# Kernel tuning notes

Measured on AMD Instinct MI355X. Metric: run time of the kernel, lower is better.

Reference implementation:

```python
import jax, jax.numpy as jnp
import numpy as np

B, C, H, W, L = 2, 64, 48, 48, 48
GH, GW, GL = 24, 24, 24  # gating signal at half resolution


def setup_inputs() -> dict:
    key = jax.random.key(0)
    k = jax.random.split(key, 6)
    x = jax.random.normal(k[0], (B, C, H, W, L), dtype=jnp.float32)
    g = jax.random.normal(k[1], (B, C, GH, GW, GL), dtype=jnp.float32)
    s = 1.0 / np.sqrt(C)
    W1 = jax.random.normal(k[2], (C, C), dtype=jnp.float32) * s  # conv1 1x1x1 weight (out,in)
    b1 = jax.random.normal(k[3], (C,), dtype=jnp.float32) * 0.01
    W2 = jax.random.normal(k[4], (C, C), dtype=jnp.float32) * s  # conv2 1x1x1 weight
    b2 = jax.random.normal(k[5], (C,), dtype=jnp.float32) * 0.01
    return {"x": x, "g": g, "W1": W1, "b1": b1, "W2": W2, "b2": b2}


def _conv1x1(v, Wm, b):
    # 1x1x1 Conv3d == channel-mixing matmul
    return jnp.einsum('bchwl,oc->bohwl', v, Wm) + b[None, :, None, None, None]


def reference(x, g, W1, b1, W2, b2):
    theta_x = _conv1x1(x, W1, b1)                       # (B, C, H, W, L)
    theta_g = _conv1x1(g, W2, b2)                       # (B, C, GH, GW, GL)
    # F.upsample(mode='trilinear', align_corners=False) -> half-pixel trilinear resize
    theta_g = jax.image.resize(theta_g, (B, C, H, W, L), method='trilinear')

    # spatially-normalized elementwise gate
    theta_c = theta_x * theta_g
    theta_c = theta_c - jnp.min(theta_c)                # global min over whole tensor
    theta_c = theta_c / jnp.sum(theta_c, axis=(2, 3, 4), keepdims=True)
    p = theta_c * x

    # channel-channel attention per (b,h,w), contracting over L
    theta_c_d = jnp.einsum('bihwl,bjhwl->bhwij', theta_x, theta_g)  # (B,H,W,C,C)
    theta_c_d = theta_c_d - jnp.min(theta_c_d)
    theta_c_d = theta_c_d / jnp.sum(theta_c_d, axis=(1, 2, 3, 4), keepdims=True)
    d = jnp.einsum('bchwl,bhwcj->bjhwl', x, theta_c_d)  # (B, C, H, W, L)
    return (p, d)
```

## Files before the change

kernel.cpp:

```cpp
#include <hip/hip_runtime.h>

#define Bb 2
#define Cc 64
#define Hh 48
#define Ww 48
#define Ll 48
#define HWc (Hh*Ww)
#define HWL (HWc*Ll)
#define GHh 24
#define SG (GHh*GHh*GHh)
#define NBLK (Bb*HWc)
#define CNT1f 110592.0f
#define CNT2f 9437184.0f

__device__ __forceinline__ void interp1(int i, int& a, int& b, float& f){
  float src = i*0.5f - 0.25f;
  float fl = floorf(src);
  f = src - fl;
  int i0 = (int)fl;
  a = i0 < 0 ? 0 : i0;
  int i1 = i0 + 1;
  b = i1 > (GHh-1) ? (GHh-1) : i1;
}

__global__ __launch_bounds__(256) void conv_k(const float* __restrict__ in,
    const float* __restrict__ Wm, const float* __restrict__ bias,
    float* __restrict__ out, int S){
  __shared__ __align__(16) float Wl[64][68];
  __shared__ __align__(16) float xl[64][68];
  int t = threadIdx.x;
  int ntile = S >> 6;
  int b  = blockIdx.x / ntile;
  int s0 = (blockIdx.x % ntile) << 6;
  for (int q = t; q < 4096; q += 256){
    int o = q >> 6, c = q & 63;
    Wl[c][o] = Wm[q];
  }
  const float* inb = in + (size_t)b*Cc*S + s0;
  for (int q = t; q < 1024; q += 256){
    int c = q >> 4, v = (q & 15) << 2;
    float4 val = *(const float4*)(inb + (size_t)c*S + v);
    *(float4*)&xl[c][v] = val;
  }
  __syncthreads();
  int o0 = (t & 15) << 2, s1 = (t >> 4) << 2;
  float a00=0,a01=0,a02=0,a03=0,a10=0,a11=0,a12=0,a13=0;
  float a20=0,a21=0,a22=0,a23=0,a30=0,a31=0,a32=0,a33=0;
  #pragma unroll 8
  for (int c = 0; c < 64; ++c){
    float4 wv = *(const float4*)&Wl[c][o0];
    float4 xv = *(const float4*)&xl[c][s1];
    a00 += wv.x*xv.x; a01 += wv.x*xv.y; a02 += wv.x*xv.z; a03 += wv.x*xv.w;
    a10 += wv.y*xv.x; a11 += wv.y*xv.y; a12 += wv.y*xv.z; a13 += wv.y*xv.w;
    a20 += wv.z*xv.x; a21 += wv.z*xv.y; a22 += wv.z*xv.z; a23 += wv.z*xv.w;
    a30 += wv.w*xv.x; a31 += wv.w*xv.y; a32 += wv.w*xv.z; a33 += wv.w*xv.w;
  }
  float* ob = out + (size_t)b*Cc*S + s0 + s1;
  float b0 = bias[o0+0], b1v = bias[o0+1], b2v = bias[o0+2], b3 = bias[o0+3];
  { float4 r = make_float4(a00+b0,a01+b0,a02+b0,a03+b0); *(float4*)(ob + (size_t)(o0+0)*S) = r; }
  { float4 r = make_float4(a10+b1v,a11+b1v,a12+b1v,a13+b1v); *(float4*)(ob + (size_t)(o0+1)*S) = r; }
  { float4 r = make_float4(a20+b2v,a21+b2v,a22+b2v,a23+b2v); *(float4*)(ob + (size_t)(o0+2)*S) = r; }
  { float4 r = make_float4(a30+b3,a31+b3,a32+b3,a33+b3); *(float4*)(ob + (size_t)(o0+3)*S) = r; }
}

__device__ __forceinline__ void g_fold(const float* __restrict__ txt,
    float* __restrict__ G, int t){
  int c = t >> 2, kb = (t & 3)*6;
  const float* T = &txt[c*52];
  #pragma unroll
  for (int i = 0; i < 6; ++i){
    int k = kb + i;
    float v;
    if (k == 0)       v = T[0] + 0.75f*T[1] + 0.25f*T[2];
    else if (k == 23) v = 0.25f*T[45] + 0.75f*T[46] + T[47];
    else              v = 0.25f*T[2*k-1] + 0.75f*T[2*k]
                        + 0.75f*T[2*k+1] + 0.25f*T[2*k+2];
    G[k*68 + c] = v;
  }
}

__device__ __forceinline__ void gather_m(const float* __restrict__ gb,
    float* __restrict__ M, int t, int ha, int hb, int wa, int wb,
    float fh, float fw){
  float omh = 1.f - fh, omw = 1.f - fw;
  for (int u = t; u < 384; u += 256){
    int c = u / 6, s4 = (u % 6) << 2;
    const float* gc = gb + (size_t)c*SG;
    float4 vaa = *(const float4*)(gc + ha*576 + wa*24 + s4);
    float4 vba = *(const float4*)(gc + hb*576 + wa*24 + s4);
    float4 vab = *(const float4*)(gc + ha*576 + wb*24 + s4);
    float4 vbb = *(const float4*)(gc + hb*576 + wb*24 + s4);
    M[(s4+0)*68 + c] = omw*(omh*vaa.x + fh*vba.x) + fw*(omh*vab.x + fh*vbb.x);
    M[(s4+1)*68 + c] = omw*(omh*vaa.y + fh*vba.y) + fw*(omh*vab.y + fh*vbb.y);
    M[(s4+2)*68 + c] = omw*(omh*vaa.z + fh*vba.z) + fw*(omh*vab.z + fh*vbb.z);
    M[(s4+3)*68 + c] = omw*(omh*vaa.w + fh*vba.w) + fw*(omh*vab.w + fh*vbb.w);
  }
}

__global__ __launch_bounds__(256) void reduce_k(const float* __restrict__ tx,
    const float* __restrict__ tgh, float* __restrict__ part_row,
    float* __restrict__ pm1, float* __restrict__ pm2, float* __restrict__ ps2){
  __shared__ __align__(16) float sh[7224];
  float* txt = sh;
  float* M   = sh + 3328;
  float* G   = sh + 4960;
  float* red = sh + 6592;
  float* CM  = sh + 7104;
  float* SX  = sh + 7128;
  float* sxg = sh + 7176;
  int t = threadIdx.x;
  int bIdx = blockIdx.x;
  int b = bIdx / HWc, hw = bIdx % HWc;
  int h = hw / Ww, w = hw % Ww;
  int ha, hb; float fh; interp1(h, ha, hb, fh);
  int wa, wb; float fw; interp1(w, wa, wb, fw);
  const float* txb = tx + ((size_t)b*Cc*HWc + hw)*Ll;
  #pragma unroll
  for (int k = 0; k < 3; ++k){
    int q = t + (k << 8);
    int c = q / 12, v = (q % 12) << 2;
    *(float4*)&txt[c*52+v] = *(const float4*)(txb + (size_t)c*HWL + v);
  }
  gather_m(tgh + (size_t)b*Cc*SG, M, t, ha, hb, wa, wb, fh, fw);
  __syncthreads();
  g_fold(txt, G, t);
  if (t < 24){
    float s = 0.f;
    #pragma unroll 8
    for (int c = 0; c < 64; ++c) s += M[t*68 + c];
    CM[t] = s;
  }
  if (t >= 192 && t < 240){
    int l = t - 192;
    float s = 0.f;
    #pragma unroll 8
    for (int c = 0; c < 64; ++c) s += txt[c*52 + l];
    SX[l] = s;
  }
  __syncthreads();
  int c = t & 63, lg = t >> 6;
  float pmin = 3.4e38f;
  const float* Trow = &txt[c*52];
  #pragma unroll
  for (int li = 0; li < 12; ++li){
    int l = lg*12 + li;
    int la, lb; float fl; interp1(l, la, lb, fl);
    float tgv = (1.f-fl)*M[la*68 + c] + fl*M[lb*68 + c];
    pmin = fminf(pmin, Trow[l]*tgv);
  }
  if (t < 48){
    int la, lb; float fl; interp1(t, la, lb, fl);
    sxg[t] = SX[t] * ((1.f-fl)*CM[la] + fl*CM[lb]);
  }
  int i0 = (t & 15) << 2, j0 = (t >> 4) << 2;
  float a00=0,a01=0,a02=0,a03=0,a10=0,a11=0,a12=0,a13=0;
  float a20=0,a21=0,a22=0,a23=0,a30=0,a31=0,a32=0,a33=0;
  #pragma unroll 4
  for (int k = 0; k < 24; ++k){
    float4 gv = *(const float4*)&G[k*68 + i0];
    float4 mv = *(const float4*)&M[k*68 + j0];
    a00 += gv.x*mv.x; a01 += gv.x*mv.y; a02 += gv.x*mv.z; a03 += gv.x*mv.w;
    a10 += gv.y*mv.x; a11 += gv.y*mv.y; a12 += gv.y*mv.z; a13 += gv.y*mv.w;
    a20 += gv.z*mv.x; a21 += gv.z*mv.y; a22 += gv.z*mv.z; a23 += gv.z*mv.w;
    a30 += gv.w*mv.x; a31 += gv.w*mv.y; a32 += gv.w*mv.z; a33 += gv.w*mv.w;
  }
  float amin = fminf(fminf(fminf(a00,a01),fminf(a02,a03)),
               fminf(fminf(fminf(a10,a11),fminf(a12,a13)),
               fminf(fminf(fminf(a20,a21),fminf(a22,a23)),
                     fminf(fminf(a30,a31),fminf(a32,a33)))));
  if ((t & 15) == (t >> 4)){
    float* pr = part_row + (size_t)bIdx*64 + i0;
    pr[0] = a00; pr[1] = a11; pr[2] = a22; pr[3] = a33;
  }
  red[t] = pmin; red[256+t] = amin;
  __syncthreads();
  if (t < 128){
    red[t] = fminf(red[t], red[t+128]);
    red[256+t] = fminf(red[256+t], red[384+t]);
  }
  __syncthreads();
  if (t < 64){
    float v1 = fminf(red[t], red[t+64]);
    float v2 = fminf(red[256+t], red[320+t]);
    #pragma unroll
    for (int off = 32; off; off >>= 1){
      v1 = fminf(v1, __shfl_down(v1, off));
      v2 = fminf(v2, __shfl_down(v2, off));
    }
    if (t == 0){
      pm1[bIdx] = v1; pm2[bIdx] = v2;
      float tot = 0.f;
      #pragma unroll
      for (int l = 0; l < 48; ++l) tot += sxg[l];
      ps2[bIdx] = tot;
    }
  }
}

__global__ __launch_bounds__(256) void reduce2_k(const float* __restrict__ part_row,
    const float* __restrict__ pm1, const float* __restrict__ pm2,
    const float* __restrict__ ps2, float* __restrict__ rowsum,
    float* __restrict__ gmin, float* __restrict__ s2v){
  __shared__ float red[512];
  int t = threadIdx.x, blk = blockIdx.x;
  if (blk < 128){
    int b = blk >> 6, c = blk & 63;
    const float* src = part_row + (size_t)b*HWc*64 + c;
    float s = 0.f;
    #pragma unroll
    for (int k = 0; k < 9; ++k){
      int i = t + (k << 8);
      s += src[(size_t)i*64];
    }
    red[t] = s; __syncthreads();
    for (int sgap = 128; sgap >= 64; sgap >>= 1){
      if (t < sgap) red[t] += red[t+sgap];
      __syncthreads();
    }
    if (t < 64){
      float v = red[t];
      #pragma unroll
      for (int off = 32; off; off >>= 1) v += __shfl_down(v, off);
      if (t == 0) rowsum[blk] = v;
    }
  } else if (blk == 128){
    float m1 = 3.4e38f, m2 = 3.4e38f;
    for (int i = t; i < NBLK; i += 256){ m1 = fminf(m1, pm1[i]); m2 = fminf(m2, pm2[i]); }
    red[t] = m1; red[256+t] = m2; __syncthreads();
    for (int s = 128; s >= 1; s >>= 1){
      if (t < s){ red[t] = fminf(red[t], red[t+s]); red[256+t] = fminf(red[256+t], red[256+t+s]); }
      __syncthreads();
    }
    if (t == 0){ gmin[0] = red[0]; gmin[1] = red[256]; }
  } else {
    float sa = 0.f, sb = 0.f;
    for (int i = t; i < HWc; i += 256){ sa += ps2[i]; sb += ps2[HWc + i]; }
    red[t] = sa; red[256+t] = sb; __syncthreads();
    for (int s = 128; s >= 1; s >>= 1){
      if (t < s){ red[t] += red[t+s]; red[256+t] += red[256+t+s]; }
      __syncthreads();
    }
    if (t == 0){ s2v[0] = red[0]; s2v[1] = red[256]; }
  }
}

__global__ __launch_bounds__(256) void final_k(const float* __restrict__ x,
    const float* __restrict__ tx, const float* __restrict__ tgh,
    const float* __restrict__ gmin, const float* __restrict__ rowsum,
    const float* __restrict__ s2v, float* __restrict__ outp, float* __restrict__ outd){
  __shared__ __align__(16) float sh[10032];
  float* txt = sh;
  float* xs  = sh + 3328;
  float* M   = sh + 6656;
  float* G   = sh + 8288;
  float* iv1 = sh + 9920;
  float* Xs  = sh + 9984;
  int t = threadIdx.x;
  int bIdx = blockIdx.x;
  int b = bIdx / HWc, hw = bIdx % HWc;
  int h = hw / Ww, w = hw % Ww;
  int ha, hb; float fh; interp1(h, ha, hb, fh);
  int wa, wb; float fw; interp1(w, wa, wb, fw);
  size_t sbase = ((size_t)b*Cc*HWc + hw)*Ll;
  const float* txb = tx + sbase;
  const float* xb  = x  + sbase;
  float m1 = gmin[0], m2 = gmin[1];
  #pragma unroll
  for (int k = 0; k < 3; ++k){
    int q = t + (k << 8);
    int c = q / 12, v = (q % 12) << 2;
    *(float4*)&txt[c*52+v] = *(const float4*)(txb + (size_t)c*HWL + v);
    *(float4*)&xs [c*52+v] = *(const float4*)(xb  + (size_t)c*HWL + v);
  }
  gather_m(tgh + (size_t)b*Cc*SG, M, t, ha, hb, wa, wb, fh, fw);
  __syncthreads();
  g_fold(txt, G, t);
  if (t < 64) iv1[t] = 1.f/(rowsum[b*64 + t] - m1*CNT1f);
  if (t >= 192 && t < 240){
    int l = t - 192;
    float s = 0.f;
    #pragma unroll 8
    for (int c = 0; c < 64; ++c) s += xs[c*52 + l];
    Xs[l] = s;
  }
  float invd2 = 1.f/(s2v[b] - m2*CNT2f);
  __syncthreads();
  #pragma unroll
  for (int k = 0; k < 3; ++k){
    int q = t + (k << 8);
    int c = q / 12, l4 = (q % 12) << 2;
    float4 a  = *(const float4*)&txt[c*52+l4];
    float4 xv = *(const float4*)&xs [c*52+l4];
    float s = iv1[c];
    float4 r;
    {
      int la, lb; float fl; interp1(l4+0, la, lb, fl);
      float tgv = (1.f-fl)*M[la*68+c] + fl*M[lb*68+c];
      r.x = (a.x*tgv - m1)*s*xv.x;
    }
    {
      int la, lb; float fl; interp1(l4+1, la, lb, fl);
      float tgv = (1.f-fl)*M[la*68+c] + fl*M[lb*68+c];
      r.y = (a.y*tgv - m1)*s*xv.y;
    }
    {
      int la, lb; float fl; interp1(l4+2, la, lb, fl);
      float tgv = (1.f-fl)*M[la*68+c] + fl*M[lb*68+c];
      r.z = (a.z*tgv - m1)*s*xv.z;
    }
    {
      int la, lb; float fl; interp1(l4+3, la, lb, fl);
      float tgv = (1.f-fl)*M[la*68+c] + fl*M[lb*68+c];
      r.w = (a.w*tgv - m1)*s*xv.w;
    }
    *(float4*)(outp + sbase + (size_t)c*HWL + l4) = r;
  }
  __syncthreads();
  float* P = txt;
  if (t < 192){
    int k0 = t >> 3, l0 = (t & 7)*6;
    float c0=0,c1=0,c2=0,c3=0,c4=0,c5=0;
    const float* Gr = &G[k0*68];
    #pragma unroll 8
    for (int i = 0; i < 64; ++i){
      float gv = Gr[i];
      const float* xr = &xs[i*52 + l0];
      c0 += gv*xr[0]; c1 += gv*xr[1]; c2 += gv*xr[2];
      c3 += gv*xr[3]; c4 += gv*xr[4]; c5 += gv*xr[5];
    }
    float* pr = &P[k0*52 + l0];
    pr[0]=c0; pr[1]=c1; pr[2]=c2; pr[3]=c3; pr[4]=c4; pr[5]=c5;
  }
  __syncthreads();
  {
    int j0 = (t >> 4) << 2, l0 = (t & 15)*3;
    float d00=0,d01=0,d02=0,d10=0,d11=0,d12=0;
    float d20=0,d21=0,d22=0,d30=0,d31=0,d32=0;
    #pragma unroll 4
    for (int k = 0; k < 24; ++k){
      float4 mv = *(const float4*)&M[k*68 + j0];
      const float* pr = &P[k*52 + l0];
      float p0 = pr[0], p1 = pr[1], p2 = pr[2];
      d00 += mv.x*p0; d01 += mv.x*p1; d02 += mv.x*p2;
      d10 += mv.y*p0; d11 += mv.y*p1; d12 += mv.y*p2;
      d20 += mv.z*p0; d21 += mv.z*p1; d22 += mv.z*p2;
      d30 += mv.w*p0; d31 += mv.w*p1; d32 += mv.w*p2;
    }
    float x0 = m2*Xs[l0+0], x1 = m2*Xs[l0+1], x2 = m2*Xs[l0+2];
    float* o0 = outd + sbase + (size_t)(j0+0)*HWL + l0;
    float* o1 = outd + sbase + (size_t)(j0+1)*HWL + l0;
    float* o2 = outd + sbase + (size_t)(j0+2)*HWL + l0;
    float* o3 = outd + sbase + (size_t)(j0+3)*HWL + l0;
    o0[0]=(d00-x0)*invd2; o0[1]=(d01-x1)*invd2; o0[2]=(d02-x2)*invd2;
    o1[0]=(d10-x0)*invd2; o1[1]=(d11-x1)*invd2; o1[2]=(d12-x2)*invd2;
    o2[0]=(d20-x0)*invd2; o2[1]=(d21-x1)*invd2; o2[2]=(d22-x2)*invd2;
    o3[0]=(d30-x0)*invd2; o3[1]=(d31-x1)*invd2; o3[2]=(d32-x2)*invd2;
  }
}

extern "C" void kernel_launch(void* const* d_in, const int* in_sizes, int n_in,
                              void* d_out, int out_size, void* d_ws, size_t ws_size,
                              hipStream_t stream){
  (void)in_sizes; (void)n_in; (void)out_size; (void)ws_size;
  const float* x  = (const float*)d_in[0];
  const float* g  = (const float*)d_in[1];
  const float* W1 = (const float*)d_in[2];
  const float* b1 = (const float*)d_in[3];
  const float* W2 = (const float*)d_in[4];
  const float* b2 = (const float*)d_in[5];
  float* outp = (float*)d_out;
  float* outd = outp + (size_t)Bb*Cc*HWL;
  float* ws   = (float*)d_ws;
  float* txw    = ws;
  float* tghw   = txw + (size_t)Bb*Cc*HWL;
  float* part_row = tghw + (size_t)Bb*Cc*SG;
  float* pm1 = part_row + (size_t)NBLK*64;
  float* pm2 = pm1 + NBLK;
  float* ps2 = pm2 + NBLK;
  float* rowsum = ps2 + NBLK;
  float* gmin = rowsum + 128;
  float* s2v  = gmin + 2;

  hipLaunchKernelGGL(conv_k, dim3(Bb*(SG/64)), dim3(256), 0, stream, g, W2, b2, tghw, SG);
  hipLaunchKernelGGL(conv_k, dim3(Bb*(HWL/64)), dim3(256), 0, stream, x, W1, b1, txw, HWL);
  hipLaunchKernelGGL(reduce_k, dim3(NBLK), dim3(256), 0, stream, txw, tghw,
                     part_row, pm1, pm2, ps2);
  hipLaunchKernelGGL(reduce2_k, dim3(130), dim3(256), 0, stream, part_row, pm1, pm2, ps2,
                     rowsum, gmin, s2v);
  hipLaunchKernelGGL(final_k, dim3(NBLK), dim3(256), 0, stream, x, txw, tghw,
                     gmin, rowsum, s2v, outp, outd);
}
```

Baseline: 310.7 us.

## Fuse full-resolution conv1 into reduce and final kernels, recomputing theta_x per site

Drops the separate conv_k launch that wrote theta_x (about 28 MB) to the workspace. Both reduce_k and final_k now load x and a transposed copy of W1 into shared memory and recompute the 64x48 channel-mixing matmul for each (b,h,w) site. The global write and the two later reads of theta_x go away. In exchange each site does the conv twice, uses more shared memory per block (which may lower occupancy), and adds extra barriers.

```diff
diff --git a/kernel.cpp b/kernel.cpp
--- a/kernel.cpp
+++ b/kernel.cpp
@@ -61,22 +61,6 @@
   { float4 r = make_float4(a10+b1v,a11+b1v,a12+b1v,a13+b1v); *(float4*)(ob + (size_t)(o0+1)*S) = r; }
   { float4 r = make_float4(a20+b2v,a21+b2v,a22+b2v,a23+b2v); *(float4*)(ob + (size_t)(o0+2)*S) = r; }
   { float4 r = make_float4(a30+b3,a31+b3,a32+b3,a33+b3); *(float4*)(ob + (size_t)(o0+3)*S) = r; }
-}
-
-__device__ __forceinline__ void g_fold(const float* __restrict__ txt,
-    float* __restrict__ G, int t){
-  int c = t >> 2, kb = (t & 3)*6;
-  const float* T = &txt[c*52];
-  #pragma unroll
-  for (int i = 0; i < 6; ++i){
-    int k = kb + i;
-    float v;
-    if (k == 0)       v = T[0] + 0.75f*T[1] + 0.25f*T[2];
-    else if (k == 23) v = 0.25f*T[45] + 0.75f*T[46] + T[47];
-    else              v = 0.25f*T[2*k-1] + 0.75f*T[2*k]
-                        + 0.75f*T[2*k+1] + 0.25f*T[2*k+2];
-    G[k*68 + c] = v;
-  }
 }
 
 __device__ __forceinline__ void gather_m(const float* __restrict__ gb,
@@ -97,50 +81,107 @@
   }
 }
 
-__global__ __launch_bounds__(256) void reduce_k(const float* __restrict__ tx,
+__device__ __forceinline__ void g_fold(const float* __restrict__ txt,
+    float* __restrict__ G, int t){
+  int c = t >> 2, kb = (t & 3)*6;
+  const float* T = &txt[c*72];
+  #pragma unroll
+  for (int i = 0; i < 6; ++i){
+    int k = kb + i;
+    float v;
+    if (k == 0)       v = T[0] + 0.75f*T[1] + 0.25f*T[2];
+    else if (k == 23) v = 0.25f*T[45] + 0.75f*T[46] + T[47];
+    else              v = 0.25f*T[2*k-1] + 0.75f*T[2*k]
+                        + 0.75f*T[2*k+1] + 0.25f*T[2*k+2];
+    G[k*68 + c] = v;
+  }
+}
+
+__device__ __forceinline__ void site_conv(const float* __restrict__ xs,
+    const float* __restrict__ Wl, const float* __restrict__ b1,
+    int c0, int l0, float4 acc[4]){
+  acc[0] = make_float4(0.f,0.f,0.f,0.f);
+  acc[1] = make_float4(0.f,0.f,0.f,0.f);
+  acc[2] = make_float4(0.f,0.f,0.f,0.f);
+  acc[3] = make_float4(0.f,0.f,0.f,0.f);
+  #pragma unroll 8
+  for (int cc = 0; cc < 64; ++cc){
+    float4 wv = *(const float4*)&Wl[cc*72 + c0];
+    float4 xv = *(const float4*)&xs[cc*52 + l0];
+    acc[0].x += wv.x*xv.x; acc[0].y += wv.x*xv.y; acc[0].z += wv.x*xv.z; acc[0].w += wv.x*xv.w;
+    acc[1].x += wv.y*xv.x; acc[1].y += wv.y*xv.y; acc[1].z += wv.y*xv.z; acc[1].w += wv.y*xv.w;
+    acc[2].x += wv.z*xv.x; acc[2].y += wv.z*xv.y; acc[2].z += wv.z*xv.z; acc[2].w += wv.z*xv.w;
+    acc[3].x += wv.w*xv.x; acc[3].y += wv.w*xv.y; acc[3].z += wv.w*xv.z; acc[3].w += wv.w*xv.w;
+  }
+  float b0 = b1[c0+0], bb1 = b1[c0+1], b2 = b1[c0+2], b3 = b1[c0+3];
+  acc[0].x += b0;  acc[0].y += b0;  acc[0].z += b0;  acc[0].w += b0;
+  acc[1].x += bb1; acc[1].y += bb1; acc[1].z += bb1; acc[1].w += bb1;
+  acc[2].x += b2;  acc[2].y += b2;  acc[2].z += b2;  acc[2].w += b2;
+  acc[3].x += b3;  acc[3].y += b3;  acc[3].z += b3;  acc[3].w += b3;
+}
+
+__global__ __launch_bounds__(256) void reduce_k(const float* __restrict__ x,
+    const float* __restrict__ W1, const float* __restrict__ b1,
     const float* __restrict__ tgh, float* __restrict__ part_row,
     float* __restrict__ pm1, float* __restrict__ pm2, float* __restrict__ ps2){
-  __shared__ __align__(16) float sh[7224];
-  float* txt = sh;
-  float* M   = sh + 3328;
-  float* G   = sh + 4960;
-  float* red = sh + 6592;
-  float* CM  = sh + 7104;
-  float* SX  = sh + 7128;
-  float* sxg = sh + 7176;
+  __shared__ __align__(16) float sh[11832];
+  float* xs  = sh;
+  float* Wt  = sh + 3328;
+  float* M   = sh + 7936;
+  float* G   = sh + 9568;
+  float* red = sh + 11200;
+  float* CM  = sh + 11712;
+  float* SX  = sh + 11736;
+  float* sxg = sh + 11784;
   int t = threadIdx.x;
   int bIdx = blockIdx.x;
   int b = bIdx / HWc, hw = bIdx % HWc;
   int h = hw / Ww, w = hw % Ww;
   int ha, hb; float fh; interp1(h, ha, hb, fh);
   int wa, wb; float fw; interp1(w, wa, wb, fw);
-  const float* txb = tx + ((size_t)b*Cc*HWc + hw)*Ll;
+  const float* xb = x + ((size_t)b*Cc*HWc + hw)*Ll;
   #pragma unroll
   for (int k = 0; k < 3; ++k){
     int q = t + (k << 8);
     int c = q / 12, v = (q % 12) << 2;
-    *(float4*)&txt[c*52+v] = *(const float4*)(txb + (size_t)c*HWL + v);
+    *(float4*)&xs[c*52+v] = *(const float4*)(xb + (size_t)c*HWL + v);
+  }
+  for (int q = t; q < 4096; q += 256){
+    int o = q >> 6, c = q & 63;
+    Wt[c*72 + o] = W1[q];
   }
   gather_m(tgh + (size_t)b*Cc*SG, M, t, ha, hb, wa, wb, fh, fw);
   __syncthreads();
-  g_fold(txt, G, t);
-  if (t < 24){
+  int c0 = (t & 15) << 2, l0q = (t >> 4) << 2;
+  float4 acc[4];
+  if (t < 192) site_conv(xs, Wt, b1, c0, l0q, acc);
+  if (t >= 192 && t < 216){
+    int k = t - 192;
     float s = 0.f;
     #pragma unroll 8
-    for (int c = 0; c < 64; ++c) s += M[t*68 + c];
-    CM[t] = s;
-  }
+    for (int c = 0; c < 64; ++c) s += M[k*68 + c];
+    CM[k] = s;
+  }
+  __syncthreads();
+  if (t < 192){
+    *(float4*)&Wt[(c0+0)*72 + l0q] = acc[0];
+    *(float4*)&Wt[(c0+1)*72 + l0q] = acc[1];
+    *(float4*)&Wt[(c0+2)*72 + l0q] = acc[2];
+    *(float4*)&Wt[(c0+3)*72 + l0q] = acc[3];
+  }
+  __syncthreads();
+  g_fold(Wt, G, t);
   if (t >= 192 && t < 240){
     int l = t - 192;
     float s = 0.f;
     #pragma unroll 8
-    for (int c = 0; c < 64; ++c) s += txt[c*52 + l];
+    for (int c = 0; c < 64; ++c) s += Wt[c*72 + l];
     SX[l] = s;
   }
   __syncthreads();
   int c = t & 63, lg = t >> 6;
   float pmin = 3.4e38f;
-  const float* Trow = &txt[c*52];
+  const float* Trow = &Wt[c*72];
   #pragma unroll
   for (int li = 0; li < 12; ++li){
     int l = lg*12 + li;
@@ -245,16 +286,17 @@
 }
 
 __global__ __launch_bounds__(256) void final_k(const float* __restrict__ x,
-    const float* __restrict__ tx, const float* __restrict__ tgh,
-    const float* __restrict__ gmin, const float* __restrict__ rowsum,
-    const float* __restrict__ s2v, float* __restrict__ outp, float* __restrict__ outd){
-  __shared__ __align__(16) float sh[10032];
-  float* txt = sh;
-  float* xs  = sh + 3328;
-  float* M   = sh + 6656;
-  float* G   = sh + 8288;
-  float* iv1 = sh + 9920;
-  float* Xs  = sh + 9984;
+    const float* __restrict__ W1, const float* __restrict__ b1,
+    const float* __restrict__ tgh, const float* __restrict__ gmin,
+    const float* __restrict__ rowsum, const float* __restrict__ s2v,
+    float* __restrict__ outp, float* __restrict__ outd){
+  __shared__ __align__(16) float sh[11312];
+  float* xs  = sh;
+  float* Wt  = sh + 3328;
+  float* M   = sh + 7936;
+  float* G   = sh + 9568;
+  float* iv1 = sh + 11200;
+  float* Xs  = sh + 11264;
   int t = threadIdx.x;
   int bIdx = blockIdx.x;
   int b = bIdx / HWc, hw = bIdx % HWc;
@@ -262,20 +304,25 @@
   int ha, hb; float fh; interp1(h, ha, hb, fh);
   int wa, wb; float fw; interp1(w, wa, wb, fw);
   size_t sbase = ((size_t)b*Cc*HWc + hw)*Ll;
-  const float* txb = tx + sbase;
-  const float* xb  = x  + sbase;
+  const float* xb = x + sbase;
   float m1 = gmin[0], m2 = gmin[1];
   #pragma unroll
   for (int k = 0; k < 3; ++k){
     int q = t + (k << 8);
     int c = q / 12, v = (q % 12) << 2;
-    *(float4*)&txt[c*52+v] = *(const float4*)(txb + (size_t)c*HWL + v);
-    *(float4*)&xs [c*52+v] = *(const float4*)(xb  + (size_t)c*HWL + v);
+    *(float4*)&xs[c*52+v] = *(const float4*)(xb + (size_t)c*HWL + v);
+  }
+  for (int q = t; q < 4096; q += 256){
+    int o = q >> 6, c = q & 63;
+    Wt[c*72 + o] = W1[q];
   }
   gather_m(tgh + (size_t)b*Cc*SG, M, t, ha, hb, wa, wb, fh, fw);
-  __syncthreads();
-  g_fold(txt, G, t);
   if (t < 64) iv1[t] = 1.f/(rowsum[b*64 + t] - m1*CNT1f);
+  float invd2 = 1.f/(s2v[b] - m2*CNT2f);
+  __syncthreads();
+  int c0 = (t & 15) << 2, l0q = (t >> 4) << 2;
+  float4 acc[4];
+  if (t < 192) site_conv(xs, Wt, b1, c0, l0q, acc);
   if (t >= 192 && t < 240){
     int l = t - 192;
     float s = 0.f;
@@ -283,14 +330,22 @@
     for (int c = 0; c < 64; ++c) s += xs[c*52 + l];
     Xs[l] = s;
   }
-  float invd2 = 1.f/(s2v[b] - m2*CNT2f);
+  __syncthreads();
+  if (t < 192){
+    *(float4*)&Wt[(c0+0)*72 + l0q] = acc[0];
+    *(float4*)&Wt[(c0+1)*72 + l0q] = acc[1];
+    *(float4*)&Wt[(c0+2)*72 + l0q] = acc[2];
+    *(float4*)&Wt[(c0+3)*72 + l0q] = acc[3];
+  }
+  __syncthreads();
+  g_fold(Wt, G, t);
   __syncthreads();
   #pragma unroll
   for (int k = 0; k < 3; ++k){
     int q = t + (k << 8);
     int c = q / 12, l4 = (q % 12) << 2;
-    float4 a  = *(const float4*)&txt[c*52+l4];
-    float4 xv = *(const float4*)&xs [c*52+l4];
+    float4 a  = *(const float4*)&Wt[c*72+l4];
+    float4 xv = *(const float4*)&xs[c*52+l4];
     float s = iv1[c];
     float4 r;
     {
@@ -316,20 +371,20 @@
     *(float4*)(outp + sbase + (size_t)c*HWL + l4) = r;
   }
   __syncthreads();
-  float* P = txt;
+  float* P = Wt;
   if (t < 192){
     int k0 = t >> 3, l0 = (t & 7)*6;
-    float c0=0,c1=0,c2=0,c3=0,c4=0,c5=0;
+    float p0=0,p1=0,p2=0,p3=0,p4=0,p5=0;
     const float* Gr = &G[k0*68];
     #pragma unroll 8
     for (int i = 0; i < 64; ++i){
       float gv = Gr[i];
       const float* xr = &xs[i*52 + l0];
-      c0 += gv*xr[0]; c1 += gv*xr[1]; c2 += gv*xr[2];
-      c3 += gv*xr[3]; c4 += gv*xr[4]; c5 += gv*xr[5];
+      p0 += gv*xr[0]; p1 += gv*xr[1]; p2 += gv*xr[2];
+      p3 += gv*xr[3]; p4 += gv*xr[4]; p5 += gv*xr[5];
     }
     float* pr = &P[k0*52 + l0];
-    pr[0]=c0; pr[1]=c1; pr[2]=c2; pr[3]=c3; pr[4]=c4; pr[5]=c5;
+    pr[0]=p0; pr[1]=p1; pr[2]=p2; pr[3]=p3; pr[4]=p4; pr[5]=p5;
   }
   __syncthreads();
   {
@@ -371,8 +426,7 @@
   float* outp = (float*)d_out;
   float* outd = outp + (size_t)Bb*Cc*HWL;
   float* ws   = (float*)d_ws;
-  float* txw    = ws;
-  float* tghw   = txw + (size_t)Bb*Cc*HWL;
+  float* tghw   = ws;
   float* part_row = tghw + (size_t)Bb*Cc*SG;
   float* pm1 = part_row + (size_t)NBLK*64;
   float* pm2 = pm1 + NBLK;
@@ -382,11 +436,10 @@
   float* s2v  = gmin + 2;
 
   hipLaunchKernelGGL(conv_k, dim3(Bb*(SG/64)), dim3(256), 0, stream, g, W2, b2, tghw, SG);
-  hipLaunchKernelGGL(conv_k, dim3(Bb*(HWL/64)), dim3(256), 0, stream, x, W1, b1, txw, HWL);
-  hipLaunchKernelGGL(reduce_k, dim3(NBLK), dim3(256), 0, stream, txw, tghw,
+  hipLaunchKernelGGL(reduce_k, dim3(NBLK), dim3(256), 0, stream, x, W1, b1, tghw,
                      part_row, pm1, pm2, ps2);
   hipLaunchKernelGGL(reduce2_k, dim3(130), dim3(256), 0, stream, part_row, pm1, pm2, ps2,
                      rowsum, gmin, s2v);
-  hipLaunchKernelGGL(final_k, dim3(NBLK), dim3(256), 0, stream, x, txw, tghw,
+  hipLaunchKernelGGL(final_k, dim3(NBLK), dim3(256), 0, stream, x, W1, b1, tghw,
                      gmin, rowsum, s2v, outp, outd);
 }
```

Measured after the change: 317.4 us. 1.02x slower.

## Cache per-site interpolated gate and folded G from reduce kernel for final kernel

Applied to the files above, without the earlier changes.

The reduce kernel now writes its per-(b,h,w) interpolated gate matrix M and folded G matrix to workspace. The final kernel loads them instead of re-gathering the gating tensor and recomputing the fold. The final kernel also reads theta_x directly from global memory rather than staging it in shared memory, and uses closed-form L-axis interpolation weights (0.25/0.75). This cuts recomputation and shared memory use in the final kernel at the cost of about 2x1536 floats of extra global writes and reads per site. The reduce loop's L index is also rotated by channel, likely to spread shared-memory bank accesses.

```diff
diff --git a/kernel.cpp b/kernel.cpp
--- a/kernel.cpp
+++ b/kernel.cpp
@@ -21,6 +21,13 @@
   a = i0 < 0 ? 0 : i0;
   int i1 = i0 + 1;
   b = i1 > (GHh-1) ? (GHh-1) : i1;
+}
+
+__device__ __forceinline__ void ltaps(int l, int& a, int& b, float& f){
+  int i0 = (l - 1) >> 1;
+  a = i0 < 0 ? 0 : i0;
+  b = i0 + 1 > 23 ? 23 : i0 + 1;
+  f = (l & 1) ? 0.25f : 0.75f;
 }
 
 __global__ __launch_bounds__(256) void conv_k(const float* __restrict__ in,
@@ -98,7 +105,8 @@
 }
 
 __global__ __launch_bounds__(256) void reduce_k(const float* __restrict__ tx,
-    const float* __restrict__ tgh, float* __restrict__ part_row,
+    const float* __restrict__ tgh, float* __restrict__ msite,
+    float* __restrict__ gsite, float* __restrict__ part_row,
     float* __restrict__ pm1, float* __restrict__ pm2, float* __restrict__ ps2){
   __shared__ __align__(16) float sh[7224];
   float* txt = sh;
@@ -143,14 +151,28 @@
   const float* Trow = &txt[c*52];
   #pragma unroll
   for (int li = 0; li < 12; ++li){
-    int l = lg*12 + li;
-    int la, lb; float fl; interp1(l, la, lb, fl);
+    int l0r = lg*12 + li + c;
+    int l = l0r >= 96 ? l0r - 96 : (l0r >= 48 ? l0r - 48 : l0r);
+    int la, lb; float fl; ltaps(l, la, lb, fl);
     float tgv = (1.f-fl)*M[la*68 + c] + fl*M[lb*68 + c];
     pmin = fminf(pmin, Trow[l]*tgv);
   }
   if (t < 48){
-    int la, lb; float fl; interp1(t, la, lb, fl);
+    int la, lb; float fl; ltaps(t, la, lb, fl);
     sxg[t] = SX[t] * ((1.f-fl)*CM[la] + fl*CM[lb]);
+  }
+  float* msb = msite + (size_t)bIdx*1536;
+  float* gsb = gsite + (size_t)bIdx*1536;
+  for (int u = t; u < 384; u += 256){
+    int k = u >> 4, c4 = (u & 15) << 2;
+    float4 mv;
+    mv.x = M[k*68+c4+0]; mv.y = M[k*68+c4+1];
+    mv.z = M[k*68+c4+2]; mv.w = M[k*68+c4+3];
+    *(float4*)(msb + (u << 2)) = mv;
+    float4 gv;
+    gv.x = G[k*68+c4+0]; gv.y = G[k*68+c4+1];
+    gv.z = G[k*68+c4+2]; gv.w = G[k*68+c4+3];
+    *(float4*)(gsb + (u << 2)) = gv;
   }
   int i0 = (t & 15) << 2, j0 = (t >> 4) << 2;
   float a00=0,a01=0,a02=0,a03=0,a10=0,a11=0,a12=0,a13=0;
@@ -245,78 +267,40 @@
 }
 
 __global__ __launch_bounds__(256) void final_k(const float* __restrict__ x,
-    const float* __restrict__ tx, const float* __restrict__ tgh,
-    const float* __restrict__ gmin, const float* __restrict__ rowsum,
-    const float* __restrict__ s2v, float* __restrict__ outp, float* __restrict__ outd){
-  __shared__ __align__(16) float sh[10032];
-  float* txt = sh;
-  float* xs  = sh + 3328;
-  float* M   = sh + 6656;
-  float* G   = sh + 8288;
-  float* iv1 = sh + 9920;
-  float* Xs  = sh + 9984;
+    const float* __restrict__ tx, const float* __restrict__ msite,
+    const float* __restrict__ gsite, const float* __restrict__ gmin,
+    const float* __restrict__ rowsum, const float* __restrict__ s2v,
+    float* __restrict__ outp, float* __restrict__ outd){
+  __shared__ __align__(16) float sh[7952];
+  float* xs  = sh;
+  float* M   = sh + 3328;
+  float* G   = sh + 4960;
+  float* P   = sh + 6592;
+  float* iv1 = sh + 7840;
+  float* Xs  = sh + 7904;
   int t = threadIdx.x;
   int bIdx = blockIdx.x;
   int b = bIdx / HWc, hw = bIdx % HWc;
-  int h = hw / Ww, w = hw % Ww;
-  int ha, hb; float fh; interp1(h, ha, hb, fh);
-  int wa, wb; float fw; interp1(w, wa, wb, fw);
   size_t sbase = ((size_t)b*Cc*HWc + hw)*Ll;
+  const float* xb  = x  + sbase;
   const float* txb = tx + sbase;
-  const float* xb  = x  + sbase;
   float m1 = gmin[0], m2 = gmin[1];
   #pragma unroll
   for (int k = 0; k < 3; ++k){
     int q = t + (k << 8);
     int c = q / 12, v = (q % 12) << 2;
-    *(float4*)&txt[c*52+v] = *(const float4*)(txb + (size_t)c*HWL + v);
-    *(float4*)&xs [c*52+v] = *(const float4*)(xb  + (size_t)c*HWL + v);
-  }
-  gather_m(tgh + (size_t)b*Cc*SG, M, t, ha, hb, wa, wb, fh, fw);
-  __syncthreads();
-  g_fold(txt, G, t);
+    *(float4*)&xs[c*52+v] = *(const float4*)(xb + (size_t)c*HWL + v);
+  }
+  const float* msb = msite + (size_t)bIdx*1536;
+  const float* gsb = gsite + (size_t)bIdx*1536;
+  for (int u = t; u < 384; u += 256){
+    int k = u >> 4, c4 = (u & 15) << 2;
+    *(float4*)&M[k*68 + c4] = *(const float4*)(msb + (u << 2));
+    *(float4*)&G[k*68 + c4] = *(const float4*)(gsb + (u << 2));
+  }
   if (t < 64) iv1[t] = 1.f/(rowsum[b*64 + t] - m1*CNT1f);
-  if (t >= 192 && t < 240){
-    int l = t - 192;
-    float s = 0.f;
-    #pragma unroll 8
-    for (int c = 0; c < 64; ++c) s += xs[c*52 + l];
-    Xs[l] = s;
-  }
   float invd2 = 1.f/(s2v[b] - m2*CNT2f);
   __syncthreads();
-  #pragma unroll
-  for (int k = 0; k < 3; ++k){
-    int q = t + (k << 8);
-    int c = q / 12, l4 = (q % 12) << 2;
-    float4 a  = *(const float4*)&txt[c*52+l4];
-    float4 xv = *(const float4*)&xs [c*52+l4];
-    float s = iv1[c];
-    float4 r;
-    {
-      int la, lb; float fl; interp1(l4+0, la, lb, fl);
-      float tgv = (1.f-fl)*M[la*68+c] + fl*M[lb*68+c];
-      r.x = (a.x*tgv - m1)*s*xv.x;
-    }
-    {
-      int la, lb; float fl; interp1(l4+1, la, lb, fl);
-      float tgv = (1.f-fl)*M[la*68+c] + fl*M[lb*68+c];
-      r.y = (a.y*tgv - m1)*s*xv.y;
-    }
-    {
-      int la, lb; float fl; interp1(l4+2, la, lb, fl);
-      float tgv = (1.f-fl)*M[la*68+c] + fl*M[lb*68+c];
-      r.z = (a.z*tgv - m1)*s*xv.z;
-    }
-    {
-      int la, lb; float fl; interp1(l4+3, la, lb, fl);
-      float tgv = (1.f-fl)*M[la*68+c] + fl*M[lb*68+c];
-      r.w = (a.w*tgv - m1)*s*xv.w;
-    }
-    *(float4*)(outp + sbase + (size_t)c*HWL + l4) = r;
-  }
-  __syncthreads();
-  float* P = txt;
   if (t < 192){
     int k0 = t >> 3, l0 = (t & 7)*6;
     float c0=0,c1=0,c2=0,c3=0,c4=0,c5=0;
@@ -330,6 +314,34 @@
     }
     float* pr = &P[k0*52 + l0];
     pr[0]=c0; pr[1]=c1; pr[2]=c2; pr[3]=c3; pr[4]=c4; pr[5]=c5;
+  } else if (t < 240){
+    int l = t - 192;
+    float s = 0.f;
+    #pragma unroll 8
+    for (int c = 0; c < 64; ++c) s += xs[c*52 + l];
+    Xs[l] = s;
+  }
+  __syncthreads();
+  #pragma unroll
+  for (int k = 0; k < 3; ++k){
+    int q = t + (k << 8);
+    int c = q / 12, l4 = (q % 12) << 2;
+    int hh = l4 >> 1;
+    int im1 = hh - 1 < 0 ? 0 : hh - 1;
+    int ip2 = hh + 2 > 23 ? 23 : hh + 2;
+    float Mm1 = M[im1*68 + c];
+    float M0  = M[hh*68 + c];
+    float M1  = M[(hh+1)*68 + c];
+    float M2  = M[ip2*68 + c];
+    float4 a  = *(const float4*)(txb + (size_t)c*HWL + l4);
+    float4 xv = *(const float4*)&xs[c*52 + l4];
+    float s = iv1[c];
+    float4 r;
+    r.x = (a.x*(0.25f*Mm1 + 0.75f*M0) - m1)*s*xv.x;
+    r.y = (a.y*(0.75f*M0  + 0.25f*M1) - m1)*s*xv.y;
+    r.z = (a.z*(0.25f*M0  + 0.75f*M1) - m1)*s*xv.z;
+    r.w = (a.w*(0.75f*M1  + 0.25f*M2) - m1)*s*xv.w;
+    *(float4*)(outp + sbase + (size_t)c*HWL + l4) = r;
   }
   __syncthreads();
   {
@@ -373,7 +385,9 @@
   float* ws   = (float*)d_ws;
   float* txw    = ws;
   float* tghw   = txw + (size_t)Bb*Cc*HWL;
-  float* part_row = tghw + (size_t)Bb*Cc*SG;
+  float* msite  = tghw + (size_t)Bb*Cc*SG;
+  float* gsite  = msite + (size_t)NBLK*1536;
+  float* part_row = gsite + (size_t)NBLK*1536;
   float* pm1 = part_row + (size_t)NBLK*64;
   float* pm2 = pm1 + NBLK;
   float* ps2 = pm2 + NBLK;
@@ -383,10 +397,10 @@
 
   hipLaunchKernelGGL(conv_k, dim3(Bb*(SG/64)), dim3(256), 0, stream, g, W2, b2, tghw, SG);
   hipLaunchKernelGGL(conv_k, dim3(Bb*(HWL/64)), dim3(256), 0, stream, x, W1, b1, txw, HWL);
-  hipLaunchKernelGGL(reduce_k, dim3(NBLK), dim3(256), 0, stream, txw, tghw,
+  hipLaunchKernelGGL(reduce_k, dim3(NBLK), dim3(256), 0, stream, txw, tghw, msite, gsite,
                      part_row, pm1, pm2, ps2);
   hipLaunchKernelGGL(reduce2_k, dim3(130), dim3(256), 0, stream, part_row, pm1, pm2, ps2,
                      rowsum, gmin, s2v);
-  hipLaunchKernelGGL(final_k, dim3(NBLK), dim3(256), 0, stream, x, txw, tghw,
+  hipLaunchKernelGGL(final_k, dim3(NBLK), dim3(256), 0, stream, x, txw, msite, gsite,
                      gmin, rowsum, s2v, outp, outd);
 }
```

Result: slower. 321.0 us (+3.3%).
